# Kernel optimization log

Measured on AMD Instinct MI355X. Metric: run time of the kernel, lower is better.

The kernel has to match this reference:

```python
import jax, jax.numpy as jnp
import numpy as np

T, B, I, H, E, C = 256, 64, 1024, 1024, 4, 128
STDV = 1.0 / np.sqrt(H)


def setup_inputs() -> dict:
    key = jax.random.key(0)
    ks = jax.random.split(key, 8)
    x_seq = jax.random.normal(ks[0], (T, B, I), dtype=jnp.float32)
    h0 = jnp.zeros((1, B, H), dtype=jnp.float32)
    c0 = jnp.zeros((1, B, H), dtype=jnp.float32)
    coef = jax.random.uniform(ks[1], (B, E), dtype=jnp.float32)
    # expert params (uniform(-stdv, stdv) init as in the torch module)
    u = lambda k, shp: jax.random.uniform(k, shp, dtype=jnp.float32, minval=-STDV, maxval=STDV)
    Wi = u(ks[2], (E, 4 * H, I))
    bi = u(ks[3], (E, 4 * H))
    Wh = u(ks[4], (E, 4 * H, H))
    bh = u(ks[5], (E, 4 * H))
    Wo = u(ks[6], (E, C, H))
    bo = u(ks[7], (E, C))
    return {"x_seq": x_seq, "h0": h0, "c0": c0, "coef": coef,
            "Wi": Wi, "bi": bi, "Wh": Wh, "bh": bh, "Wo": Wo, "bo": bo}


def reference(x_seq, h0, c0, coef, Wi, bi, Wh, bh, Wo, bo):
    # MoO with IDGate == per-sample convex combination of expert linear outputs,
    # which equals a linear layer with per-sample mixed weights.
    # Precompute mixed input projections for all timesteps: [T,B,4H]
    xi = jnp.einsum('tbi,eoi,be->tbo', x_seq, Wi, coef) + coef @ bi
    # Per-sample mixed hidden weights: [B,4H,H] and bias [B,4H]
    Whm = jnp.einsum('eoi,be->boi', Wh, coef)
    bhm = coef @ bh

    def step(carry, xg):
        h, c = carry
        gates = xg + jnp.einsum('bi,boi->bo', h, Whm) + bhm  # [B,4H]
        ig, fg, gg, og = jnp.split(gates, 4, axis=-1)  # i,f,g,o order as in torch chunk
        c = jax.nn.sigmoid(fg) * c + jax.nn.sigmoid(ig) * jnp.tanh(gg)
        h = jax.nn.sigmoid(og) * jnp.tanh(c)
        return (h, c), h

    (hT, cT), hs = jax.lax.scan(step, (h0[0], c0[0]), xi)  # hs: [T,B,H]
    # h2o: mixed output projection (activation is identity, dropout p=0)
    out = jnp.einsum('tbh,ech,be->tbc', hs, Wo, coef) + coef @ bo  # [T,B,C]
    return out, hT[None], cT[None]
```

## Files before the change

### kernel.cpp

```cpp
#include <hip/hip_runtime.h>
#include <hip/hip_fp16.h>
#include <cstdint>

#define T_  256
#define B_  64
#define I_  1024
#define H_  1024
#define E_  4
#define C_  128
#define G4  4096

typedef _Float16 f16;
typedef _Float16 f16x8 __attribute__((ext_vector_type(8)));
typedef float    f32x4 __attribute__((ext_vector_type(4)));

__device__ __forceinline__ float sigmoidf_(float x) { return 1.f / (1.f + __expf(-x)); }

__global__ void k_f32_to_f16(const float* __restrict__ src, f16* __restrict__ dst, int n8) {
    int i = blockIdx.x * blockDim.x + threadIdx.x;
    int stride = gridDim.x * blockDim.x;
    for (; i < n8; i += stride) {
        const float4* s = reinterpret_cast<const float4*>(src) + (size_t)i * 2;
        float4 a = s[0], b = s[1];
        f16x8 v = { (f16)a.x, (f16)a.y, (f16)a.z, (f16)a.w,
                    (f16)b.x, (f16)b.y, (f16)b.z, (f16)b.w };
        *reinterpret_cast<f16x8*>(dst + (size_t)i * 8) = v;
    }
}

__global__ void k_mix_biases(const float* __restrict__ coef, const float* __restrict__ bi,
                             const float* __restrict__ bh, const float* __restrict__ bo,
                             float* __restrict__ gbias, float* __restrict__ bom) {
    int idx = blockIdx.x * blockDim.x + threadIdx.x;
    int stride = gridDim.x * blockDim.x;
    for (int i = idx; i < B_ * G4; i += stride) {
        int b = i >> 12, o = i & (G4 - 1);
        float s = 0.f;
#pragma unroll
        for (int e = 0; e < 4; ++e) s += coef[b * 4 + e] * (bi[e * G4 + o] + bh[e * G4 + o]);
        gbias[i] = s;
    }
    for (int i = idx; i < B_ * C_; i += stride) {
        int b = i >> 7, c = i & (C_ - 1);
        float s = 0.f;
#pragma unroll
        for (int e = 0; e < 4; ++e) s += coef[b * 4 + e] * bo[e * C_ + c];
        bom[i] = s;
    }
}

__global__ void k_init_h0h(const float* __restrict__ h0, f16* __restrict__ h0h) {
    int i = blockIdx.x * blockDim.x + threadIdx.x;
    if (i < B_ * H_) h0h[i] = (f16)h0[i];
}

template<bool XF16, bool WF16>
__global__ __launch_bounds__(256, 1) void k_xi_gemm(
        const f16* __restrict__ xh, const float* __restrict__ xf,
        const f16* __restrict__ Wih, const float* __restrict__ Wif,
        const float* __restrict__ coef, const float* __restrict__ gbias,
        f16* __restrict__ xi) {
    __shared__ f16 As[256 * 72];
    __shared__ f16 Bs[128 * 72];
    const int nt = blockIdx.x;
    const int b  = blockIdx.y;
    const int tid = threadIdx.x;
    const int lane = tid & 63, wave = tid >> 6;
    const int wr = wave >> 1, wc = wave & 1;

    float cf[4];
#pragma unroll
    for (int e = 0; e < 4; ++e) cf[e] = coef[b * 4 + e];

    f32x4 acc[8][4];
#pragma unroll
    for (int mi = 0; mi < 8; ++mi)
#pragma unroll
        for (int ni = 0; ni < 4; ++ni) acc[mi][ni] = 0.f;

    for (int kk = 0; kk < I_; kk += 64) {
        __syncthreads();
#pragma unroll
        for (int it = 0; it < 8; ++it) {
            int chunk = it * 256 + tid;
            int row = chunk >> 3, c8 = chunk & 7;
            if constexpr (XF16) {
                *reinterpret_cast<f16x8*>(&As[row * 72 + c8 * 8]) =
                    *reinterpret_cast<const f16x8*>(&xh[((size_t)row * B_ + b) * I_ + kk + c8 * 8]);
            } else {
                const float4* p = reinterpret_cast<const float4*>(&xf[((size_t)row * B_ + b) * I_ + kk + c8 * 8]);
                float4 a = p[0], bq = p[1];
                f16x8 v = { (f16)a.x, (f16)a.y, (f16)a.z, (f16)a.w,
                            (f16)bq.x, (f16)bq.y, (f16)bq.z, (f16)bq.w };
                *reinterpret_cast<f16x8*>(&As[row * 72 + c8 * 8]) = v;
            }
        }
#pragma unroll
        for (int it = 0; it < 4; ++it) {
            int chunk = it * 256 + tid;
            int n = chunk >> 3, c8 = chunk & 7;
            if constexpr (WF16) {
                size_t base = ((size_t)(nt * 128 + n)) * I_ + kk + c8 * 8;
                f16 c0 = (f16)cf[0], c1 = (f16)cf[1], c2 = (f16)cf[2], c3 = (f16)cf[3];
                f16x8 w0 = *reinterpret_cast<const f16x8*>(&Wih[base]);
                f16x8 w1 = *reinterpret_cast<const f16x8*>(&Wih[base + (size_t)1 * G4 * I_]);
                f16x8 w2 = *reinterpret_cast<const f16x8*>(&Wih[base + (size_t)2 * G4 * I_]);
                f16x8 w3 = *reinterpret_cast<const f16x8*>(&Wih[base + (size_t)3 * G4 * I_]);
                f16x8 m = w0 * c0 + w1 * c1 + w2 * c2 + w3 * c3;
                *reinterpret_cast<f16x8*>(&Bs[n * 72 + c8 * 8]) = m;
            } else {
                size_t base = ((size_t)(nt * 128 + n)) * I_ + kk + c8 * 8;
                float m[8];
#pragma unroll
                for (int j = 0; j < 8; ++j) m[j] = 0.f;
#pragma unroll
                for (int e = 0; e < 4; ++e) {
                    const float4* p = reinterpret_cast<const float4*>(&Wif[base + (size_t)e * G4 * I_]);
                    float4 a = p[0], bq = p[1];
                    m[0] += cf[e] * a.x;  m[1] += cf[e] * a.y;
                    m[2] += cf[e] * a.z;  m[3] += cf[e] * a.w;
                    m[4] += cf[e] * bq.x; m[5] += cf[e] * bq.y;
                    m[6] += cf[e] * bq.z; m[7] += cf[e] * bq.w;
                }
                f16x8 v = { (f16)m[0], (f16)m[1], (f16)m[2], (f16)m[3],
                            (f16)m[4], (f16)m[5], (f16)m[6], (f16)m[7] };
                *reinterpret_cast<f16x8*>(&Bs[n * 72 + c8 * 8]) = v;
            }
        }
        __syncthreads();
#pragma unroll
        for (int ks = 0; ks < 2; ++ks) {
            int ko = ks * 32 + (lane >> 4) * 8;
            f16x8 a[8], bb[4];
#pragma unroll
            for (int mi = 0; mi < 8; ++mi)
                a[mi] = *reinterpret_cast<const f16x8*>(&As[(wr * 128 + mi * 16 + (lane & 15)) * 72 + ko]);
#pragma unroll
            for (int ni = 0; ni < 4; ++ni)
                bb[ni] = *reinterpret_cast<const f16x8*>(&Bs[(wc * 64 + ni * 16 + (lane & 15)) * 72 + ko]);
#pragma unroll
            for (int mi = 0; mi < 8; ++mi)
#pragma unroll
                for (int ni = 0; ni < 4; ++ni)
                    acc[mi][ni] = __builtin_amdgcn_mfma_f32_16x16x32_f16(a[mi], bb[ni], acc[mi][ni], 0, 0, 0);
        }
    }
#pragma unroll
    for (int mi = 0; mi < 8; ++mi)
#pragma unroll
        for (int ni = 0; ni < 4; ++ni)
#pragma unroll
            for (int j = 0; j < 4; ++j) {
                int t = wr * 128 + mi * 16 + (lane >> 4) * 4 + j;
                int o = nt * 128 + wc * 64 + ni * 16 + (lane & 15);
                float v = acc[mi][ni][j] + gbias[b * G4 + o];
                xi[((size_t)t * B_ + b) * G4 + o] = (f16)v;
            }
}

__device__ __forceinline__ void grid_barrier3(int* __restrict__ arr, int* __restrict__ go,
                                              int t, int bid) {
    __syncthreads();
    const int tid = threadIdx.x;
    if (bid == 0) {
        if (tid >= 1 && tid < 256) {
            while (__hip_atomic_load(&arr[t * 256 + tid], __ATOMIC_RELAXED,
                                     __HIP_MEMORY_SCOPE_AGENT) == 0)
                __builtin_amdgcn_s_sleep(1);
        }
        __syncthreads();
        if (tid == 0)
            __hip_atomic_store(&go[t * 512 + 511], 1, __ATOMIC_RELEASE,
                               __HIP_MEMORY_SCOPE_AGENT);
        __syncthreads();
        if (tid < 32)
            __hip_atomic_store(&go[t * 512 + tid * 16], 1, __ATOMIC_RELAXED,
                               __HIP_MEMORY_SCOPE_AGENT);
        __syncthreads();
    } else {
        if (tid == 0) {
            __hip_atomic_store(&arr[t * 256 + bid], 1, __ATOMIC_RELEASE,
                               __HIP_MEMORY_SCOPE_AGENT);
            while (__hip_atomic_load(&go[t * 512 + (bid >> 3) * 16], __ATOMIC_RELAXED,
                                     __HIP_MEMORY_SCOPE_AGENT) == 0)
                __builtin_amdgcn_s_sleep(1);
        }
        __builtin_amdgcn_sched_barrier(0);
        __syncthreads();
    }
}

#define POOL_SZ  148480
#define AS0_OFF  131072
#define AS1_OFF  (131072 + 8192)
#define GL_OFF   131072

#define BF(KC, KS) (*reinterpret_cast<const f16x8*>(pool + wrow + (KC) * 128 + (((KS) * 64 + koff) ^ swz)))

#define PRE(KC, PF) PF = *reinterpret_cast<const f16x8*>(&hprev[(size_t)sr * hstr + (KC) * 64 + soct * 8]);

#define AFR(AOFF, AROW, KS) (*reinterpret_cast<const f16x8*>(pool + (AOFF) + (AROW) + (((KS) * 64 + koff) ^ swz)))

#define MM4(ROFF) \
    acc0 = __builtin_amdgcn_mfma_f32_16x16x32_f16(AFR(ROFF, arow0, 0), bq0, acc0, 0, 0, 0); \
    acc1 = __builtin_amdgcn_mfma_f32_16x16x32_f16(AFR(ROFF, arow1, 0), bq0, acc1, 0, 0, 0); \
    acc0 = __builtin_amdgcn_mfma_f32_16x16x32_f16(AFR(ROFF, arow0, 1), bq1, acc0, 0, 0, 0); \
    acc1 = __builtin_amdgcn_mfma_f32_16x16x32_f16(AFR(ROFF, arow1, 1), bq1, acc1, 0, 0, 0);

#define KST(KC, ROFF, WOFF, PFW) { \
    const f16x8 bq0 = BF(KC, 0), bq1 = BF(KC, 1); \
    MM4(ROFF); \
    *reinterpret_cast<f16x8*>(pool + (WOFF) + sdst) = PFW; \
    __syncthreads(); \
}
#define KSTP(KC, ROFF, WOFF, PFW, PFL) { \
    const f16x8 bq0 = BF(KC, 0), bq1 = BF(KC, 1); \
    PRE((KC) + 4, PFL); \
    MM4(ROFF); \
    *reinterpret_cast<f16x8*>(pool + (WOFF) + sdst) = PFW; \
    __syncthreads(); \
}

__global__ __launch_bounds__(512, 1) void k_rec_persist(
        const float* __restrict__ Wh, const f16* __restrict__ h0h,
        const float* __restrict__ c0, f16* xi, const float* __restrict__ coef,
        float* __restrict__ out, int* __restrict__ arr, int* __restrict__ go) {
    __shared__ __attribute__((aligned(16))) char pool[POOL_SZ];
    float* gl = reinterpret_cast<float*>(pool + GL_OFF);

    const int bid = blockIdx.x;
    const int jb = ((bid & 7) << 5) | (bid >> 3);
    const int tid = threadIdx.x, lane = tid & 63, w = tid >> 6;
    const int ex = w & 3, mh = w >> 2;
    const int l15 = lane & 15, hi8 = (lane >> 4) * 8;

    for (int i = tid; i < 8192; i += 512) {
        int r = i >> 7, oct = i & 127;
        int e = r >> 4, g = (r >> 2) & 3, c = r & 3;
        const float* src = &Wh[((size_t)e * G4 + g * H_ + jb * 4 + c) * H_ + oct * 8];
        float4 f0 = *reinterpret_cast<const float4*>(src);
        float4 f1 = *reinterpret_cast<const float4*>(src + 4);
        f16x8 v = { (f16)f0.x, (f16)f0.y, (f16)f0.z, (f16)f0.w,
                    (f16)f1.x, (f16)f1.y, (f16)f1.z, (f16)f1.w };
        int db = r * 2048 + ((oct * 16) ^ ((r & 7) << 4));
        *reinterpret_cast<f16x8*>(pool + db) = v;
    }

    const int bb = tid >> 2, cl = tid & 3;
    const int col = jb * 4 + cl;
    float c_reg = 0.f;
    float4 cf4 = {0.f, 0.f, 0.f, 0.f};
    if (tid < 256) {
        c_reg = c0[bb * H_ + col];
        cf4 = *reinterpret_cast<const float4*>(&coef[bb * 4]);
    }

    const int swz   = (l15 & 7) << 4;
    const int koff  = hi8 * 2;
    const int wrow  = (ex * 16 + l15) * 2048;
    const int arow0 = (mh * 32 + l15) * 128;
    const int arow1 = arow0 + 16 * 128;
    const int sr = tid >> 3, soct = tid & 7;
    const int sdst = sr * 128 + ((soct * 16) ^ ((sr & 7) << 4));

    __syncthreads();

    float xgc0 = 0.f, xgc1 = 0.f, xgc2 = 0.f, xgc3 = 0.f;
    if (tid < 256) {
        const f16* xp = &xi[((size_t)0 * B_ + bb) * G4 + col];
        xgc0 = (float)*reinterpret_cast<const volatile f16*>(&xp[0]);
        xgc1 = (float)xp[H_];
        xgc2 = (float)xp[2 * H_]; xgc3 = (float)xp[3 * H_];
    }

    for (int t = 0; t < T_; ++t) {
        const f16* hprev = (t == 0) ? h0h : (xi + (size_t)(t - 1) * B_ * G4);
        const size_t hstr = (t == 0) ? (size_t)H_ : (size_t)G4;

        float xgn0 = 0.f, xgn1 = 0.f, xgn2 = 0.f, xgn3 = 0.f;
        if (t + 1 < T_ && tid < 256) {
            const f16* xq = &xi[((size_t)(t + 1) * B_ + bb) * G4 + col];
            xgn0 = (float)*reinterpret_cast<const volatile f16*>(&xq[0]);
            xgn1 = (float)xq[H_];
            xgn2 = (float)xq[2 * H_]; xgn3 = (float)xq[3 * H_];
        }

        f16x8 pfa, pfb, pfc, pfd;
        PRE(0, pfa) PRE(1, pfb) PRE(2, pfc) PRE(3, pfd)
        *reinterpret_cast<f16x8*>(pool + AS0_OFF + sdst) = pfa;
        f32x4 acc0 = {0.f, 0.f, 0.f, 0.f}, acc1 = {0.f, 0.f, 0.f, 0.f};
        __syncthreads();

        KSTP(0,  AS0_OFF, AS1_OFF, pfb, pfa)
        KSTP(1,  AS1_OFF, AS0_OFF, pfc, pfb)
        KSTP(2,  AS0_OFF, AS1_OFF, pfd, pfc)
        KSTP(3,  AS1_OFF, AS0_OFF, pfa, pfd)
        KSTP(4,  AS0_OFF, AS1_OFF, pfb, pfa)
        KSTP(5,  AS1_OFF, AS0_OFF, pfc, pfb)
        KSTP(6,  AS0_OFF, AS1_OFF, pfd, pfc)
        KSTP(7,  AS1_OFF, AS0_OFF, pfa, pfd)
        KSTP(8,  AS0_OFF, AS1_OFF, pfb, pfa)
        KSTP(9,  AS1_OFF, AS0_OFF, pfc, pfb)
        KSTP(10, AS0_OFF, AS1_OFF, pfd, pfc)
        KSTP(11, AS1_OFF, AS0_OFF, pfa, pfd)
        KST(12,  AS0_OFF, AS1_OFF, pfb)
        KST(13,  AS1_OFF, AS0_OFF, pfc)
        KST(14,  AS0_OFF, AS1_OFF, pfd)
        {
            const f16x8 bq0 = BF(15, 0), bq1 = BF(15, 1);
            MM4(AS1_OFF);
            __syncthreads();
        }

#pragma unroll
        for (int j = 0; j < 4; ++j) {
            int r0 = mh * 32 + (lane >> 4) * 4 + j;
            gl[(ex * 64 + r0) * 17 + l15]      = acc0[j];
            gl[(ex * 64 + r0 + 16) * 17 + l15] = acc1[j];
        }
        __syncthreads();

        if (tid < 256) {
            float gate[4];
#pragma unroll
            for (int g = 0; g < 4; ++g) {
                int nn = g * 4 + cl;
                gate[g] = cf4.x * gl[(0 * 64 + bb) * 17 + nn] +
                          cf4.y * gl[(1 * 64 + bb) * 17 + nn] +
                          cf4.z * gl[(2 * 64 + bb) * 17 + nn] +
                          cf4.w * gl[(3 * 64 + bb) * 17 + nn];
            }
            gate[0] += xgc0; gate[1] += xgc1; gate[2] += xgc2; gate[3] += xgc3;
            float cn = sigmoidf_(gate[1]) * c_reg + sigmoidf_(gate[0]) * tanhf(gate[2]);
            float hn = sigmoidf_(gate[3]) * tanhf(cn);
            c_reg = cn;
            *reinterpret_cast<volatile f16*>(&xi[((size_t)t * B_ + bb) * G4 + col]) = (f16)hn;
            if (t == T_ - 1) {
                out[(size_t)T_ * B_ * C_ + bb * H_ + col] = hn;
                out[(size_t)T_ * B_ * C_ + B_ * H_ + bb * H_ + col] = cn;
            }
        }
        xgc0 = xgn0; xgc1 = xgn1; xgc2 = xgn2; xgc3 = xgn3;
        if (t != T_ - 1) grid_barrier3(arr, go, t, bid);
    }
}

__global__ __launch_bounds__(256, 1) void k_out_gemm(
        const f16* __restrict__ hs, const f16* __restrict__ Woh,
        const float* __restrict__ coef, const float* __restrict__ bom,
        float* __restrict__ out) {
    __shared__ f16 As[64 * 72];
    __shared__ f16 Bs[256 * 72];
    __shared__ float cfs[64][4];
    const int nt = blockIdx.x;
    const int t  = blockIdx.y;
    const int tid = threadIdx.x, lane = tid & 63, w = tid >> 6;
    cfs[tid >> 2][tid & 3] = coef[tid];

    f32x4 acc[4][4];
#pragma unroll
    for (int e = 0; e < 4; ++e)
#pragma unroll
        for (int mi = 0; mi < 4; ++mi) acc[e][mi] = 0.f;

    for (int kk = 0; kk < H_; kk += 64) {
        __syncthreads();
#pragma unroll
        for (int it = 0; it < 2; ++it) {
            int chunk = it * 256 + tid;
            int row = chunk >> 3, c8 = chunk & 7;
            *reinterpret_cast<f16x8*>(&As[row * 72 + c8 * 8]) =
                *reinterpret_cast<const f16x8*>(&hs[((size_t)t * B_ + row) * G4 + kk + c8 * 8]);
        }
#pragma unroll
        for (int it = 0; it < 8; ++it) {
            int chunk = it * 256 + tid;
            int r = chunk >> 3, c8 = chunk & 7;
            int e = r >> 6, nn = r & 63;
            size_t grow = (size_t)e * C_ + nt * 64 + nn;
            *reinterpret_cast<f16x8*>(&Bs[r * 72 + c8 * 8]) =
                *reinterpret_cast<const f16x8*>(&Woh[grow * H_ + kk + c8 * 8]);
        }
        __syncthreads();
#pragma unroll
        for (int ks = 0; ks < 2; ++ks) {
            int ko = ks * 32 + (lane >> 4) * 8;
            f16x8 a[4];
#pragma unroll
            for (int mi = 0; mi < 4; ++mi)
                a[mi] = *reinterpret_cast<const f16x8*>(&As[(mi * 16 + (lane & 15)) * 72 + ko]);
#pragma unroll
            for (int e = 0; e < 4; ++e) {
                f16x8 bf = *reinterpret_cast<const f16x8*>(&Bs[(e * 64 + w * 16 + (lane & 15)) * 72 + ko]);
#pragma unroll
                for (int mi = 0; mi < 4; ++mi)
                    acc[e][mi] = __builtin_amdgcn_mfma_f32_16x16x32_f16(a[mi], bf, acc[e][mi], 0, 0, 0);
            }
        }
    }
#pragma unroll
    for (int mi = 0; mi < 4; ++mi)
#pragma unroll
        for (int j = 0; j < 4; ++j) {
            int bb = mi * 16 + (lane >> 4) * 4 + j;
            int cc = nt * 64 + w * 16 + (lane & 15);
            float v = cfs[bb][0] * acc[0][mi][j] + cfs[bb][1] * acc[1][mi][j] +
                      cfs[bb][2] * acc[2][mi][j] + cfs[bb][3] * acc[3][mi][j];
            v += bom[bb * C_ + cc];
            out[((size_t)t * B_ + bb) * C_ + cc] = v;
        }
}

extern "C" void kernel_launch(void* const* d_in, const int* in_sizes, int n_in,
                              void* d_out, int out_size, void* d_ws, size_t ws_size,
                              hipStream_t stream) {
    const float* x    = (const float*)d_in[0];
    const float* h0   = (const float*)d_in[1];
    const float* c0   = (const float*)d_in[2];
    const float* coef = (const float*)d_in[3];
    const float* Wi   = (const float*)d_in[4];
    const float* bi   = (const float*)d_in[5];
    const float* Wh   = (const float*)d_in[6];
    const float* bh   = (const float*)d_in[7];
    const float* Wo   = (const float*)d_in[8];
    const float* bo   = (const float*)d_in[9];
    float* out = (float*)d_out;

    char* base = (char*)d_ws;
    size_t off = 0;
    auto carve = [&](size_t bytes) -> char* {
        char* r = base + off;
        off = (off + bytes + 255) & ~(size_t)255;
        return r;
    };
    const size_t SZ_XI  = (size_t)T_ * B_ * G4 * 2;
    const size_t SZ_WOH = (size_t)E_ * C_ * H_ * 2;
    const size_t SZ_ARR = (size_t)T_ * 256 * 4;
    const size_t SZ_GO  = (size_t)T_ * 512 * 4;
    const size_t SZ_WIH = (size_t)E_ * G4 * I_ * 2;
    const size_t SZ_XH  = (size_t)T_ * B_ * I_ * 2;

    f16*   xi     = (f16*)carve(SZ_XI);
    f16*   Woh    = (f16*)carve(SZ_WOH);
    f16*   h0h    = (f16*)carve((size_t)B_ * H_ * 2);
    float* gbias  = (float*)carve((size_t)B_ * G4 * 4);
    float* bom    = (float*)carve((size_t)B_ * C_ * 4);
    int*   arr    = (int*)carve(SZ_ARR);
    int*   go     = (int*)carve(SZ_GO);

    f16* Wih = nullptr;
    f16* xh  = nullptr;
    if (off + SZ_WIH + 256 <= ws_size) Wih = (f16*)carve(SZ_WIH);
    if (Wih && off + SZ_XH + 256 <= ws_size) xh = (f16*)carve(SZ_XH);
    (void)in_sizes; (void)n_in; (void)out_size;

    hipMemsetAsync(arr, 0, SZ_ARR, stream);
    hipMemsetAsync(go, 0, SZ_GO, stream);

    if (xh)  k_f32_to_f16<<<2048, 256, 0, stream>>>(x,  xh,  (T_ * B_ * I_) / 8);
    if (Wih) k_f32_to_f16<<<2048, 256, 0, stream>>>(Wi, Wih, (E_ * G4 * I_) / 8);
    k_f32_to_f16<<<512,  256, 0, stream>>>(Wo, Woh, (E_ * C_ * H_) / 8);
    k_mix_biases<<<512, 256, 0, stream>>>(coef, bi, bh, bo, gbias, bom);
    k_init_h0h<<<(B_ * H_ + 255) / 256, 256, 0, stream>>>(h0, h0h);

    dim3 gx(32, 64);
    if (xh)
        k_xi_gemm<true,  true ><<<gx, 256, 0, stream>>>(xh, nullptr, Wih, nullptr, coef, gbias, xi);
    else if (Wih)
        k_xi_gemm<false, true ><<<gx, 256, 0, stream>>>(nullptr, x, Wih, nullptr, coef, gbias, xi);
    else
        k_xi_gemm<false, false><<<gx, 256, 0, stream>>>(nullptr, x, nullptr, Wi, coef, gbias, xi);

    {
        void* args[] = { (void*)&Wh, (void*)&h0h, (void*)&c0, (void*)&xi,
                         (void*)&coef, (void*)&out, (void*)&arr, (void*)&go };
        hipLaunchCooperativeKernel((const void*)k_rec_persist, dim3(256), dim3(512),
                                   args, 0, stream);
    }

    dim3 go_(2, 256);
    k_out_gemm<<<go_, 256, 0, stream>>>(xi, Woh, coef, bom, out);
}
```

Baseline: 2.616 ms.

## Deepen h prefetch to 8 chunks and pack two columns per gate thread

Each step of the persistent recurrent kernel now issues eight h-chunk global loads up front instead of four, so more of the latency to read the previous hidden state is in flight before the MFMA loop starts. The xi prefetch for the next step is moved after those h loads. The gate epilogue now runs on 128 threads, each handling two adjacent columns with packed 32-bit atomic loads and stores instead of volatile half-precision accesses. This costs more registers per thread and halves the threads doing the pointwise math, which could lengthen the serial epilogue on the critical path.

```diff
diff --git a/kernel.cpp b/kernel.cpp
--- a/kernel.cpp
+++ b/kernel.cpp
@@ -11,10 +11,13 @@
 #define G4  4096
 
 typedef _Float16 f16;
+typedef _Float16 f16x2 __attribute__((ext_vector_type(2)));
 typedef _Float16 f16x8 __attribute__((ext_vector_type(8)));
 typedef float    f32x4 __attribute__((ext_vector_type(4)));
 
 __device__ __forceinline__ float sigmoidf_(float x) { return 1.f / (1.f + __expf(-x)); }
+
+union pk2 { uint32_t u; f16x2 h; };
 
 __global__ void k_f32_to_f16(const float* __restrict__ src, f16* __restrict__ dst, int n8) {
     int i = blockIdx.x * blockDim.x + threadIdx.x;
@@ -207,15 +210,15 @@
     acc0 = __builtin_amdgcn_mfma_f32_16x16x32_f16(AFR(ROFF, arow0, 1), bq1, acc0, 0, 0, 0); \
     acc1 = __builtin_amdgcn_mfma_f32_16x16x32_f16(AFR(ROFF, arow1, 1), bq1, acc1, 0, 0, 0);
 
-#define KST(KC, ROFF, WOFF, PFW) { \
+#define KSTP(KC, ROFF, WOFF, PFW, PFL) { \
     const f16x8 bq0 = BF(KC, 0), bq1 = BF(KC, 1); \
+    PRE((KC) + 8, PFL); \
     MM4(ROFF); \
     *reinterpret_cast<f16x8*>(pool + (WOFF) + sdst) = PFW; \
     __syncthreads(); \
 }
-#define KSTP(KC, ROFF, WOFF, PFW, PFL) { \
+#define KST(KC, ROFF, WOFF, PFW) { \
     const f16x8 bq0 = BF(KC, 0), bq1 = BF(KC, 1); \
-    PRE((KC) + 4, PFL); \
     MM4(ROFF); \
     *reinterpret_cast<f16x8*>(pool + (WOFF) + sdst) = PFW; \
     __syncthreads(); \
@@ -246,12 +249,13 @@
         *reinterpret_cast<f16x8*>(pool + db) = v;
     }
 
-    const int bb = tid >> 2, cl = tid & 3;
-    const int col = jb * 4 + cl;
-    float c_reg = 0.f;
+    const int bb = tid >> 1, pr = tid & 1;
+    const int cp0 = jb * 4 + pr * 2;
+    float c_reg0 = 0.f, c_reg1 = 0.f;
     float4 cf4 = {0.f, 0.f, 0.f, 0.f};
-    if (tid < 256) {
-        c_reg = c0[bb * H_ + col];
+    if (tid < 128) {
+        c_reg0 = c0[bb * H_ + cp0];
+        c_reg1 = c0[bb * H_ + cp0 + 1];
         cf4 = *reinterpret_cast<const float4*>(&coef[bb * 4]);
     }
 
@@ -265,28 +269,44 @@
 
     __syncthreads();
 
-    float xgc0 = 0.f, xgc1 = 0.f, xgc2 = 0.f, xgc3 = 0.f;
-    if (tid < 256) {
-        const f16* xp = &xi[((size_t)0 * B_ + bb) * G4 + col];
-        xgc0 = (float)*reinterpret_cast<const volatile f16*>(&xp[0]);
-        xgc1 = (float)xp[H_];
-        xgc2 = (float)xp[2 * H_]; xgc3 = (float)xp[3 * H_];
+    float xgc0a = 0.f, xgc0b = 0.f, xgc1a = 0.f, xgc1b = 0.f;
+    float xgc2a = 0.f, xgc2b = 0.f, xgc3a = 0.f, xgc3b = 0.f;
+    if (tid < 128) {
+        const f16* xp = &xi[((size_t)0 * B_ + bb) * G4 + cp0];
+        pk2 p0; p0.u = __hip_atomic_load(reinterpret_cast<const uint32_t*>(xp),
+                                         __ATOMIC_RELAXED, __HIP_MEMORY_SCOPE_AGENT);
+        xgc0a = (float)p0.h.x; xgc0b = (float)p0.h.y;
+        f16x2 g1 = *reinterpret_cast<const f16x2*>(xp + H_);
+        f16x2 g2 = *reinterpret_cast<const f16x2*>(xp + 2 * H_);
+        f16x2 g3 = *reinterpret_cast<const f16x2*>(xp + 3 * H_);
+        xgc1a = (float)g1.x; xgc1b = (float)g1.y;
+        xgc2a = (float)g2.x; xgc2b = (float)g2.y;
+        xgc3a = (float)g3.x; xgc3b = (float)g3.y;
     }
 
     for (int t = 0; t < T_; ++t) {
         const f16* hprev = (t == 0) ? h0h : (xi + (size_t)(t - 1) * B_ * G4);
         const size_t hstr = (t == 0) ? (size_t)H_ : (size_t)G4;
 
-        float xgn0 = 0.f, xgn1 = 0.f, xgn2 = 0.f, xgn3 = 0.f;
-        if (t + 1 < T_ && tid < 256) {
-            const f16* xq = &xi[((size_t)(t + 1) * B_ + bb) * G4 + col];
-            xgn0 = (float)*reinterpret_cast<const volatile f16*>(&xq[0]);
-            xgn1 = (float)xq[H_];
-            xgn2 = (float)xq[2 * H_]; xgn3 = (float)xq[3 * H_];
-        }
-
-        f16x8 pfa, pfb, pfc, pfd;
+        f16x8 pfa, pfb, pfc, pfd, pfe, pff, pfg, pfh;
         PRE(0, pfa) PRE(1, pfb) PRE(2, pfc) PRE(3, pfd)
+        PRE(4, pfe) PRE(5, pff) PRE(6, pfg) PRE(7, pfh)
+
+        float xgn0a = 0.f, xgn0b = 0.f, xgn1a = 0.f, xgn1b = 0.f;
+        float xgn2a = 0.f, xgn2b = 0.f, xgn3a = 0.f, xgn3b = 0.f;
+        if (t + 1 < T_ && tid < 128) {
+            const f16* xq = &xi[((size_t)(t + 1) * B_ + bb) * G4 + cp0];
+            pk2 p0; p0.u = __hip_atomic_load(reinterpret_cast<const uint32_t*>(xq),
+                                             __ATOMIC_RELAXED, __HIP_MEMORY_SCOPE_AGENT);
+            xgn0a = (float)p0.h.x; xgn0b = (float)p0.h.y;
+            f16x2 g1 = *reinterpret_cast<const f16x2*>(xq + H_);
+            f16x2 g2 = *reinterpret_cast<const f16x2*>(xq + 2 * H_);
+            f16x2 g3 = *reinterpret_cast<const f16x2*>(xq + 3 * H_);
+            xgn1a = (float)g1.x; xgn1b = (float)g1.y;
+            xgn2a = (float)g2.x; xgn2b = (float)g2.y;
+            xgn3a = (float)g3.x; xgn3b = (float)g3.y;
+        }
+
         *reinterpret_cast<f16x8*>(pool + AS0_OFF + sdst) = pfa;
         f32x4 acc0 = {0.f, 0.f, 0.f, 0.f}, acc1 = {0.f, 0.f, 0.f, 0.f};
         __syncthreads();
@@ -294,18 +314,18 @@
         KSTP(0,  AS0_OFF, AS1_OFF, pfb, pfa)
         KSTP(1,  AS1_OFF, AS0_OFF, pfc, pfb)
         KSTP(2,  AS0_OFF, AS1_OFF, pfd, pfc)
-        KSTP(3,  AS1_OFF, AS0_OFF, pfa, pfd)
-        KSTP(4,  AS0_OFF, AS1_OFF, pfb, pfa)
-        KSTP(5,  AS1_OFF, AS0_OFF, pfc, pfb)
-        KSTP(6,  AS0_OFF, AS1_OFF, pfd, pfc)
-        KSTP(7,  AS1_OFF, AS0_OFF, pfa, pfd)
-        KSTP(8,  AS0_OFF, AS1_OFF, pfb, pfa)
-        KSTP(9,  AS1_OFF, AS0_OFF, pfc, pfb)
-        KSTP(10, AS0_OFF, AS1_OFF, pfd, pfc)
-        KSTP(11, AS1_OFF, AS0_OFF, pfa, pfd)
-        KST(12,  AS0_OFF, AS1_OFF, pfb)
-        KST(13,  AS1_OFF, AS0_OFF, pfc)
-        KST(14,  AS0_OFF, AS1_OFF, pfd)
+        KSTP(3,  AS1_OFF, AS0_OFF, pfe, pfd)
+        KSTP(4,  AS0_OFF, AS1_OFF, pff, pfe)
+        KSTP(5,  AS1_OFF, AS0_OFF, pfg, pff)
+        KSTP(6,  AS0_OFF, AS1_OFF, pfh, pfg)
+        KSTP(7,  AS1_OFF, AS0_OFF, pfa, pfh)
+        KST(8,   AS0_OFF, AS1_OFF, pfb)
+        KST(9,   AS1_OFF, AS0_OFF, pfc)
+        KST(10,  AS0_OFF, AS1_OFF, pfd)
+        KST(11,  AS1_OFF, AS0_OFF, pfe)
+        KST(12,  AS0_OFF, AS1_OFF, pff)
+        KST(13,  AS1_OFF, AS0_OFF, pfg)
+        KST(14,  AS0_OFF, AS1_OFF, pfh)
         {
             const f16x8 bq0 = BF(15, 0), bq1 = BF(15, 1);
             MM4(AS1_OFF);
@@ -320,27 +340,39 @@
         }
         __syncthreads();
 
-        if (tid < 256) {
-            float gate[4];
+        if (tid < 128) {
+            float ga[4], gb[4];
 #pragma unroll
             for (int g = 0; g < 4; ++g) {
-                int nn = g * 4 + cl;
-                gate[g] = cf4.x * gl[(0 * 64 + bb) * 17 + nn] +
-                          cf4.y * gl[(1 * 64 + bb) * 17 + nn] +
-                          cf4.z * gl[(2 * 64 + bb) * 17 + nn] +
-                          cf4.w * gl[(3 * 64 + bb) * 17 + nn];
+                int nn = g * 4 + pr * 2;
+                ga[g] = cf4.x * gl[(0 * 64 + bb) * 17 + nn] +
+                        cf4.y * gl[(1 * 64 + bb) * 17 + nn] +
+                        cf4.z * gl[(2 * 64 + bb) * 17 + nn] +
+                        cf4.w * gl[(3 * 64 + bb) * 17 + nn];
+                gb[g] = cf4.x * gl[(0 * 64 + bb) * 17 + nn + 1] +
+                        cf4.y * gl[(1 * 64 + bb) * 17 + nn + 1] +
+                        cf4.z * gl[(2 * 64 + bb) * 17 + nn + 1] +
+                        cf4.w * gl[(3 * 64 + bb) * 17 + nn + 1];
             }
-            gate[0] += xgc0; gate[1] += xgc1; gate[2] += xgc2; gate[3] += xgc3;
-            float cn = sigmoidf_(gate[1]) * c_reg + sigmoidf_(gate[0]) * tanhf(gate[2]);
-            float hn = sigmoidf_(gate[3]) * tanhf(cn);
-            c_reg = cn;
-            *reinterpret_cast<volatile f16*>(&xi[((size_t)t * B_ + bb) * G4 + col]) = (f16)hn;
+            ga[0] += xgc0a; ga[1] += xgc1a; ga[2] += xgc2a; ga[3] += xgc3a;
+            gb[0] += xgc0b; gb[1] += xgc1b; gb[2] += xgc2b; gb[3] += xgc3b;
+            float cn0 = sigmoidf_(ga[1]) * c_reg0 + sigmoidf_(ga[0]) * tanhf(ga[2]);
+            float hn0 = sigmoidf_(ga[3]) * tanhf(cn0);
+            float cn1 = sigmoidf_(gb[1]) * c_reg1 + sigmoidf_(gb[0]) * tanhf(gb[2]);
+            float hn1 = sigmoidf_(gb[3]) * tanhf(cn1);
+            c_reg0 = cn0; c_reg1 = cn1;
+            pk2 st; st.h.x = (f16)hn0; st.h.y = (f16)hn1;
+            __hip_atomic_store(reinterpret_cast<uint32_t*>(&xi[((size_t)t * B_ + bb) * G4 + cp0]),
+                               st.u, __ATOMIC_RELAXED, __HIP_MEMORY_SCOPE_AGENT);
             if (t == T_ - 1) {
-                out[(size_t)T_ * B_ * C_ + bb * H_ + col] = hn;
-                out[(size_t)T_ * B_ * C_ + B_ * H_ + bb * H_ + col] = cn;
+                out[(size_t)T_ * B_ * C_ + bb * H_ + cp0]     = hn0;
+                out[(size_t)T_ * B_ * C_ + bb * H_ + cp0 + 1] = hn1;
+                out[(size_t)T_ * B_ * C_ + B_ * H_ + bb * H_ + cp0]     = cn0;
+                out[(size_t)T_ * B_ * C_ + B_ * H_ + bb * H_ + cp0 + 1] = cn1;
             }
         }
-        xgc0 = xgn0; xgc1 = xgn1; xgc2 = xgn2; xgc3 = xgn3;
+        xgc0a = xgn0a; xgc0b = xgn0b; xgc1a = xgn1a; xgc1b = xgn1b;
+        xgc2a = xgn2a; xgc2b = xgn2b; xgc3a = xgn3a; xgc3b = xgn3b;
         if (t != T_ - 1) grid_barrier3(arr, go, t, bid);
     }
 }
```

New measurement: 2.688 ms. 2.8% more time.
